# Kernel optimization log

Measured on AMD Instinct MI355X. Metric: run time of the kernel, lower is better.

## Reference

```python
import jax, jax.numpy as jnp
import numpy as np


def _make_pert(r, s):
    lin = np.linspace(-r, r, s)
    xm, ym, tm = np.meshgrid(lin, lin, lin)  # default 'xy' indexing, matches torch code
    return jnp.asarray(np.stack([xm.ravel(), ym.ravel(), tm.ravel()], axis=-1), dtype=jnp.float32)

PERTS = (_make_pert(0.01, 3), _make_pert(0.05, 5), _make_pert(0.09, 7))  # [27,3],[125,3],[343,3]

N, IN, H, HQ, FF, OUT = 4096, 3, 256, 64, 64, 3


def setup_inputs():
    key = jax.random.key(0)
    ks = jax.random.split(key, 24)

    def W(k, i, o):
        return (jax.random.normal(k, (i, o), jnp.float32) / np.sqrt(i)).astype(jnp.float32)

    one = jnp.ones((1,), jnp.float32)
    return {
        "x": jax.random.normal(ks[0], (N, 1), jnp.float32),
        "y": jax.random.normal(ks[1], (N, 1), jnp.float32),
        "t": jax.random.normal(ks[2], (N, 1), jnp.float32),
        # linear_emb: 3 -> 64 -> WaveAct -> 256
        "emb_W1": W(ks[3], IN, HQ), "emb_b1": jnp.zeros((HQ,), jnp.float32),
        "emb_wa": one, "emb_wb": one,
        "emb_W2": W(ks[4], HQ, H), "emb_b2": jnp.zeros((H,), jnp.float32),
        # multiregion_mixer: 4 -> 8 -> WaveAct -> 1
        "mix_W1": W(ks[5], 4, 8), "mix_b1": jnp.zeros((8,), jnp.float32),
        "mix_wa": one, "mix_wb": one,
        "mix_W2": W(ks[6], 8, 1), "mix_b2": jnp.zeros((1,), jnp.float32),
        "out_W0": W(ks[7], H, FF), "out_b0": jnp.zeros((FF,), jnp.float32),
        "out_wa0": one, "out_wb0": one,
        "out_Wh": jnp.stack([W(ks[8 + i], FF, FF) for i in range(3)]),
        "out_bh": jnp.zeros((3, FF), jnp.float32),
        "out_wah": jnp.ones((3, 1), jnp.float32), "out_wbh": jnp.ones((3, 1), jnp.float32),
        "out_Wf1": W(ks[11], FF, FF), "out_bf1": jnp.zeros((FF,), jnp.float32),
        "out_waf": one, "out_wbf": one,
        "out_Wf2": W(ks[12], FF, OUT), "out_bf2": jnp.zeros((OUT,), jnp.float32),
    }


def _wave(h, wa, wb):
    return wa * jnp.sin(h) + wb * jnp.cos(h)


def reference(x, y, t,
              emb_W1, emb_b1, emb_wa, emb_wb, emb_W2, emb_b2,
              mix_W1, mix_b1, mix_wa, mix_wb, mix_W2, mix_b2,
              out_W0, out_b0, out_wa0, out_wb0,
              out_Wh, out_bh, out_wah, out_wbh,
              out_Wf1, out_bf1, out_waf, out_wbf, out_Wf2, out_bf2):
    def emb(s):  # [..., 3] -> [..., 256]
        h = _wave(s @ emb_W1 + emb_b1, emb_wa, emb_wb)
        return h @ emb_W2 + emb_b2

    src = jnp.concatenate([x, y, t], axis=-1)           # [N, 3]
    feats = [emb(src)]                                   # region 1: unperturbed
    for P in PERTS:
        perturbed = src[:, None, :] + P[None, :, :]      # [N, P, 3]
        feats.append(emb(perturbed).mean(axis=1))        # [N, 256]
    stacked = jnp.stack(feats, axis=-1)                  # [N, 256, 4] (== permute(0,2,1) of stack dim=1)

    m = _wave(stacked @ mix_W1 + mix_b1, mix_wa, mix_wb) # [N, 256, 8]
    e = (m @ mix_W2 + mix_b2)[:, :, 0]                   # [N, 256]

    h = _wave(e @ out_W0 + out_b0, out_wa0, out_wb0)     # [N, 64]
    for i in range(3):                                   # fixed num_layer-1 = 3 hidden layers
        h = _wave(h @ out_Wh[i] + out_bh[i], out_wah[i], out_wbh[i])
    h = _wave(h @ out_Wf1 + out_bf1, out_waf, out_wbf)
    return h @ out_Wf2 + out_bf2                         # [N, 3]
```

## Files before the change

kernel.cpp:

```cpp
#include <hip/hip_runtime.h>

typedef _Float16 f16;
typedef _Float16 f16x8 __attribute__((ext_vector_type(8)));
typedef float v4f __attribute__((ext_vector_type(4)));

#define WS_W2T  0
#define WS_W0T  16384
#define WS_WHT  32768
#define WS_WF1T 45056
#define WS_CDW  24576
#define WS_RPHI 24768

__global__ __launch_bounds__(256) void preprocess(
    const float* __restrict__ embW1, const float* __restrict__ embW2,
    const float* __restrict__ outW0, const float* __restrict__ outWh,
    const float* __restrict__ outWf1,
    const float* __restrict__ embwa, const float* __restrict__ embwb,
    const float* __restrict__ mixwa, const float* __restrict__ mixwb,
    const float* __restrict__ outwa0, const float* __restrict__ outwb0,
    const float* __restrict__ outwah, const float* __restrict__ outwbh,
    const float* __restrict__ outwaf, const float* __restrict__ outwbf,
    f16* __restrict__ wsh)
{
    const int g = blockIdx.x * 256 + threadIdx.x;
    if (g < 16384) {
        const int c = g >> 6, k = g & 63;
        wsh[WS_W2T + g] = (f16)embW2[k*256 + c];
    } else if (g < 32768) {
        const int i = g - 16384;
        const int f = i >> 8, k = i & 255;
        wsh[WS_W0T + i] = (f16)outW0[k*64 + f];
    } else if (g < 45056) {
        const int i = g - 32768;
        const int l = i >> 12, f = (i >> 6) & 63, k = i & 63;
        wsh[WS_WHT + i] = (f16)outWh[l*4096 + k*64 + f];
    } else if (g < 49152) {
        const int i = g - 45056;
        const int f = i >> 6, k = i & 63;
        wsh[WS_WF1T + i] = (f16)outWf1[k*64 + f];
    } else if (g < 49344) {
        const int i = g - 49152;
        const int r = i >> 6, ch = i & 63;
        const float w0 = embW1[ch], w1 = embW1[64 + ch], w2 = embW1[128 + ch];
        float v;
        if (r == 0) {
            v = (1.f + 2.f*__cosf(0.01f*w0)) * (1.f + 2.f*__cosf(0.01f*w1))
              * (1.f + 2.f*__cosf(0.01f*w2)) * (1.f/27.f);
        } else if (r == 1) {
            v = (1.f + 2.f*(__cosf(0.025f*w0) + __cosf(0.05f*w0)))
              * (1.f + 2.f*(__cosf(0.025f*w1) + __cosf(0.05f*w1)))
              * (1.f + 2.f*(__cosf(0.025f*w2) + __cosf(0.05f*w2))) * (1.f/125.f);
        } else {
            v = (1.f + 2.f*(__cosf(0.03f*w0) + __cosf(0.06f*w0) + __cosf(0.09f*w0)))
              * (1.f + 2.f*(__cosf(0.03f*w1) + __cosf(0.06f*w1) + __cosf(0.09f*w1)))
              * (1.f + 2.f*(__cosf(0.03f*w2) + __cosf(0.06f*w2) + __cosf(0.09f*w2))) * (1.f/343.f);
        }
        ((float*)wsh)[WS_CDW + i] = v;
    } else if (g < 49360) {
        const int i = g - 49344;
        const int p = i >> 1;
        float wa, wb;
        switch (p) {
            case 0: wa = embwa[0];  wb = embwb[0];  break;
            case 1: wa = mixwa[0];  wb = mixwb[0];  break;
            case 2: wa = outwa0[0]; wb = outwb0[0]; break;
            case 3: case 4: case 5: wa = outwah[p-3]; wb = outwbh[p-3]; break;
            default: wa = outwaf[0]; wb = outwbf[0]; break;
        }
        const float v = (i & 1) ? atan2f(wb, wa) : sqrtf(wa*wa + wb*wb);
        ((float*)wsh)[WS_RPHI + p*2 + (i & 1)] = v;
    }
}

__global__ __launch_bounds__(256, 4) void model_mfma(
    const float* __restrict__ x, const float* __restrict__ y, const float* __restrict__ t,
    const float* __restrict__ embW1, const float* __restrict__ embb1,
    const float* __restrict__ embb2,
    const float* __restrict__ mixW1, const float* __restrict__ mixb1,
    const float* __restrict__ mixW2, const float* __restrict__ mixb2,
    const float* __restrict__ outb0, const float* __restrict__ outbh,
    const float* __restrict__ outbf1,
    const float* __restrict__ outWf2, const float* __restrict__ outbf2,
    const f16* __restrict__ wsh,
    float* __restrict__ out, int N)
{
    __shared__ __attribute__((aligned(16))) f16 sA[16*72];
    __shared__ __attribute__((aligned(16))) f16 sE[16*264];
    __shared__ __attribute__((aligned(16))) f16 sH[2][16*72];
    __shared__ float sHf[4*65];

    const int tid  = threadIdx.x;
    const int lane = tid & 63;
    const int wv   = tid >> 6;
    const int n0   = blockIdx.x * 4;
    const float* rphi = (const float*)wsh + WS_RPHI;

    {
        const int k = lane, sq = wv;
        const float w0 = embW1[k], w1 = embW1[64+k], w2 = embW1[128+k];
        const float b1 = embb1[k];
        const float* Cw = (const float*)wsh + WS_CDW;
        const float c1 = Cw[k], c2 = Cw[64+k], c3 = Cw[128+k];
        const int ns = (n0 + sq < N) ? (n0 + sq) : (N - 1);
        const float u = fmaf(x[ns], w0, fmaf(y[ns], w1, fmaf(t[ns], w2, b1)));
        const float sv = rphi[0] * __sinf(u + rphi[1]);
        f16* row = sA + (sq*4)*72 + k;
        row[0]   = (f16)sv;
        row[72]  = (f16)(sv*c1);
        row[144] = (f16)(sv*c2);
        row[216] = (f16)(sv*c3);
    }
    __syncthreads();

    const int l15 = lane & 15, qb = lane >> 4;

    {
        const f16x8 af0 = *(const f16x8*)(sA + l15*72 + qb*8);
        const f16x8 af1 = *(const f16x8*)(sA + l15*72 + 32 + qb*8);
        const float mR = rphi[2], mP = rphi[3], mb2v = mixb2[0];
        #pragma unroll
        for (int nt = 0; nt < 4; ++nt) {
            const int cb = wv*64 + nt*16;
            const f16x8 bf0 = *(const f16x8*)(wsh + WS_W2T + (cb + l15)*64 + qb*8);
            const f16x8 bf1 = *(const f16x8*)(wsh + WS_W2T + (cb + l15)*64 + 32 + qb*8);
            v4f acc = {0.f, 0.f, 0.f, 0.f};
            acc = __builtin_amdgcn_mfma_f32_16x16x32_f16(af0, bf0, acc, 0, 0, 0);
            acc = __builtin_amdgcn_mfma_f32_16x16x32_f16(af1, bf1, acc, 0, 0, 0);
            const int c = cb + l15;
            const float b2c = embb2[c];
            const float s0 = acc[0]+b2c, s1 = acc[1]+b2c, s2 = acc[2]+b2c, s3 = acc[3]+b2c;
            float ev = mb2v;
            #pragma unroll
            for (int j = 0; j < 8; ++j) {
                float p = fmaf(s0, mixW1[j],
                          fmaf(s1, mixW1[8+j],
                          fmaf(s2, mixW1[16+j],
                          fmaf(s3, mixW1[24+j], mixb1[j]))));
                ev = fmaf(mR*__sinf(p + mP), mixW2[j], ev);
            }
            sE[qb*264 + c] = (f16)ev;
        }
    }
    __syncthreads();

    const int fme = wv*16 + l15;

    {
        v4f acc = {0.f, 0.f, 0.f, 0.f};
        const f16* Ae   = sE + l15*264 + qb*8;
        const f16* W0Tg = wsh + WS_W0T + fme*256 + qb*8;
        #pragma unroll
        for (int kt = 0; kt < 8; ++kt) {
            const f16x8 af = *(const f16x8*)(Ae + kt*32);
            const f16x8 bf = *(const f16x8*)(W0Tg + kt*32);
            acc = __builtin_amdgcn_mfma_f32_16x16x32_f16(af, bf, acc, 0, 0, 0);
        }
        if (qb == 0) {
            const float b0 = outb0[fme], R = rphi[4], P = rphi[5];
            #pragma unroll
            for (int r = 0; r < 4; ++r)
                sH[0][r*72 + fme] = (f16)(R*__sinf(acc[r] + b0 + P));
        }
    }
    __syncthreads();

    int cur = 0;
    #pragma unroll
    for (int i = 0; i < 4; ++i) {
        const f16* Wg = (i < 3) ? (wsh + WS_WHT + i*4096) : (wsh + WS_WF1T);
        v4f acc = {0.f, 0.f, 0.f, 0.f};
        #pragma unroll
        for (int kt = 0; kt < 2; ++kt) {
            const f16x8 af = *(const f16x8*)(sH[cur] + l15*72 + kt*32 + qb*8);
            const f16x8 bf = *(const f16x8*)(Wg + fme*64 + kt*32 + qb*8);
            acc = __builtin_amdgcn_mfma_f32_16x16x32_f16(af, bf, acc, 0, 0, 0);
        }
        if (qb == 0) {
            float bias, R, P;
            if (i < 3) { bias = outbh[i*64 + fme]; R = rphi[6+2*i]; P = rphi[7+2*i]; }
            else       { bias = outbf1[fme];       R = rphi[12];    P = rphi[13]; }
            #pragma unroll
            for (int r = 0; r < 4; ++r) {
                const float v = R*__sinf(acc[r] + bias + P);
                if (i < 3) sH[cur^1][r*72 + fme] = (f16)v;
                else       sHf[r*65 + fme] = v;
            }
        }
        __syncthreads();
        cur ^= 1;
    }

    if (tid < 12) {
        const int s = tid / 3, o = tid - s*3;
        float a = outbf2[o];
        #pragma unroll 16
        for (int k = 0; k < 64; ++k)
            a = fmaf(sHf[s*65 + k], outWf2[k*3 + o], a);
        const int gn = n0 + s;
        if (gn < N) out[gn*3 + o] = a;
    }
}

extern "C" void kernel_launch(void* const* d_in, const int* in_sizes, int n_in,
                              void* d_out, int out_size, void* d_ws, size_t ws_size,
                              hipStream_t stream) {
    const float* x      = (const float*)d_in[0];
    const float* y      = (const float*)d_in[1];
    const float* t      = (const float*)d_in[2];
    const float* embW1  = (const float*)d_in[3];
    const float* embb1  = (const float*)d_in[4];
    const float* embwa  = (const float*)d_in[5];
    const float* embwb  = (const float*)d_in[6];
    const float* embW2  = (const float*)d_in[7];
    const float* embb2  = (const float*)d_in[8];
    const float* mixW1  = (const float*)d_in[9];
    const float* mixb1  = (const float*)d_in[10];
    const float* mixwa  = (const float*)d_in[11];
    const float* mixwb  = (const float*)d_in[12];
    const float* mixW2  = (const float*)d_in[13];
    const float* mixb2  = (const float*)d_in[14];
    const float* outW0  = (const float*)d_in[15];
    const float* outb0  = (const float*)d_in[16];
    const float* outwa0 = (const float*)d_in[17];
    const float* outwb0 = (const float*)d_in[18];
    const float* outWh  = (const float*)d_in[19];
    const float* outbh  = (const float*)d_in[20];
    const float* outwah = (const float*)d_in[21];
    const float* outwbh = (const float*)d_in[22];
    const float* outWf1 = (const float*)d_in[23];
    const float* outbf1 = (const float*)d_in[24];
    const float* outwaf = (const float*)d_in[25];
    const float* outwbf = (const float*)d_in[26];
    const float* outWf2 = (const float*)d_in[27];
    const float* outbf2 = (const float*)d_in[28];
    float* out = (float*)d_out;
    f16* wsh = (f16*)d_ws;

    const int N = in_sizes[0];

    preprocess<<<193, 256, 0, stream>>>(embW1, embW2, outW0, outWh, outWf1,
                                        embwa, embwb, mixwa, mixwb,
                                        outwa0, outwb0, outwah, outwbh,
                                        outwaf, outwbf, wsh);

    const int blocks = (N + 3) / 4;
    model_mfma<<<blocks, 256, 0, stream>>>(
        x, y, t,
        embW1, embb1, embb2,
        mixW1, mixb1, mixW2, mixb2,
        outb0, outbh, outbf1, outWf2, outbf2,
        wsh, out, N);
}
```

Measured before the change: 126.3 us.

## Run each 4-sample block with a single wavefront instead of four

Shrinks the main kernel's block from 256 threads to one 64-thread wavefront, so that one wave loops over all column tiles that four waves used to share. This is meant to remove cross-wave barrier cost and cut per-block setup overhead, since the syncthreads now cover only a single wave. In exchange, each wave does four times the serial MFMA and sin work and the per-block critical path gets longer. Occupancy now depends on how many small blocks can be resident per CU.

```diff
diff --git a/kernel.cpp b/kernel.cpp
--- a/kernel.cpp
+++ b/kernel.cpp
@@ -57,7 +57,7 @@
         }
         ((float*)wsh)[WS_CDW + i] = v;
     } else if (g < 49360) {
-        const int i = g - 49344;
+        const int i = g - 49152 - 192;
         const int p = i >> 1;
         float wa, wb;
         switch (p) {
@@ -72,7 +72,7 @@
     }
 }
 
-__global__ __launch_bounds__(256, 4) void model_mfma(
+__global__ __launch_bounds__(64) void model_mfma(
     const float* __restrict__ x, const float* __restrict__ y, const float* __restrict__ t,
     const float* __restrict__ embW1, const float* __restrict__ embb1,
     const float* __restrict__ embb2,
@@ -89,26 +89,28 @@
     __shared__ __attribute__((aligned(16))) f16 sH[2][16*72];
     __shared__ float sHf[4*65];
 
-    const int tid  = threadIdx.x;
-    const int lane = tid & 63;
-    const int wv   = tid >> 6;
+    const int lane = threadIdx.x;
     const int n0   = blockIdx.x * 4;
     const float* rphi = (const float*)wsh + WS_RPHI;
 
     {
-        const int k = lane, sq = wv;
+        const int k = lane;
         const float w0 = embW1[k], w1 = embW1[64+k], w2 = embW1[128+k];
         const float b1 = embb1[k];
         const float* Cw = (const float*)wsh + WS_CDW;
         const float c1 = Cw[k], c2 = Cw[64+k], c3 = Cw[128+k];
-        const int ns = (n0 + sq < N) ? (n0 + sq) : (N - 1);
-        const float u = fmaf(x[ns], w0, fmaf(y[ns], w1, fmaf(t[ns], w2, b1)));
-        const float sv = rphi[0] * __sinf(u + rphi[1]);
-        f16* row = sA + (sq*4)*72 + k;
-        row[0]   = (f16)sv;
-        row[72]  = (f16)(sv*c1);
-        row[144] = (f16)(sv*c2);
-        row[216] = (f16)(sv*c3);
+        const float Re = rphi[0], Pe = rphi[1];
+        #pragma unroll
+        for (int sq = 0; sq < 4; ++sq) {
+            const int ns = (n0 + sq < N) ? (n0 + sq) : (N - 1);
+            const float u = fmaf(x[ns], w0, fmaf(y[ns], w1, fmaf(t[ns], w2, b1)));
+            const float sv = Re * __sinf(u + Pe);
+            f16* row = sA + (sq*4)*72 + k;
+            row[0]   = (f16)sv;
+            row[72]  = (f16)(sv*c1);
+            row[144] = (f16)(sv*c2);
+            row[216] = (f16)(sv*c3);
+        }
     }
     __syncthreads();
 
@@ -118,9 +120,9 @@
         const f16x8 af0 = *(const f16x8*)(sA + l15*72 + qb*8);
         const f16x8 af1 = *(const f16x8*)(sA + l15*72 + 32 + qb*8);
         const float mR = rphi[2], mP = rphi[3], mb2v = mixb2[0];
-        #pragma unroll
-        for (int nt = 0; nt < 4; ++nt) {
-            const int cb = wv*64 + nt*16;
+        #pragma unroll 4
+        for (int nt = 0; nt < 16; ++nt) {
+            const int cb = nt*16;
             const f16x8 bf0 = *(const f16x8*)(wsh + WS_W2T + (cb + l15)*64 + qb*8);
             const f16x8 bf1 = *(const f16x8*)(wsh + WS_W2T + (cb + l15)*64 + 32 + qb*8);
             v4f acc = {0.f, 0.f, 0.f, 0.f};
@@ -143,23 +145,26 @@
     }
     __syncthreads();
 
-    const int fme = wv*16 + l15;
-
     {
-        v4f acc = {0.f, 0.f, 0.f, 0.f};
-        const f16* Ae   = sE + l15*264 + qb*8;
-        const f16* W0Tg = wsh + WS_W0T + fme*256 + qb*8;
+        const float R = rphi[4], P = rphi[5];
         #pragma unroll
-        for (int kt = 0; kt < 8; ++kt) {
-            const f16x8 af = *(const f16x8*)(Ae + kt*32);
-            const f16x8 bf = *(const f16x8*)(W0Tg + kt*32);
-            acc = __builtin_amdgcn_mfma_f32_16x16x32_f16(af, bf, acc, 0, 0, 0);
-        }
-        if (qb == 0) {
-            const float b0 = outb0[fme], R = rphi[4], P = rphi[5];
+        for (int ft = 0; ft < 4; ++ft) {
+            const int fme = ft*16 + l15;
+            v4f acc = {0.f, 0.f, 0.f, 0.f};
+            const f16* Ae   = sE + l15*264 + qb*8;
+            const f16* W0Tg = wsh + WS_W0T + fme*256 + qb*8;
             #pragma unroll
-            for (int r = 0; r < 4; ++r)
-                sH[0][r*72 + fme] = (f16)(R*__sinf(acc[r] + b0 + P));
+            for (int kt = 0; kt < 8; ++kt) {
+                const f16x8 af = *(const f16x8*)(Ae + kt*32);
+                const f16x8 bf = *(const f16x8*)(W0Tg + kt*32);
+                acc = __builtin_amdgcn_mfma_f32_16x16x32_f16(af, bf, acc, 0, 0, 0);
+            }
+            if (qb == 0) {
+                const float b0 = outb0[fme];
+                #pragma unroll
+                for (int r = 0; r < 4; ++r)
+                    sH[0][r*72 + fme] = (f16)(R*__sinf(acc[r] + b0 + P));
+            }
         }
     }
     __syncthreads();
@@ -168,30 +173,34 @@
     #pragma unroll
     for (int i = 0; i < 4; ++i) {
         const f16* Wg = (i < 3) ? (wsh + WS_WHT + i*4096) : (wsh + WS_WF1T);
-        v4f acc = {0.f, 0.f, 0.f, 0.f};
         #pragma unroll
-        for (int kt = 0; kt < 2; ++kt) {
-            const f16x8 af = *(const f16x8*)(sH[cur] + l15*72 + kt*32 + qb*8);
-            const f16x8 bf = *(const f16x8*)(Wg + fme*64 + kt*32 + qb*8);
-            acc = __builtin_amdgcn_mfma_f32_16x16x32_f16(af, bf, acc, 0, 0, 0);
-        }
-        if (qb == 0) {
-            float bias, R, P;
-            if (i < 3) { bias = outbh[i*64 + fme]; R = rphi[6+2*i]; P = rphi[7+2*i]; }
-            else       { bias = outbf1[fme];       R = rphi[12];    P = rphi[13]; }
+        for (int ft = 0; ft < 4; ++ft) {
+            const int fme = ft*16 + l15;
+            v4f acc = {0.f, 0.f, 0.f, 0.f};
             #pragma unroll
-            for (int r = 0; r < 4; ++r) {
-                const float v = R*__sinf(acc[r] + bias + P);
-                if (i < 3) sH[cur^1][r*72 + fme] = (f16)v;
-                else       sHf[r*65 + fme] = v;
+            for (int kt = 0; kt < 2; ++kt) {
+                const f16x8 af = *(const f16x8*)(sH[cur] + l15*72 + kt*32 + qb*8);
+                const f16x8 bf = *(const f16x8*)(Wg + fme*64 + kt*32 + qb*8);
+                acc = __builtin_amdgcn_mfma_f32_16x16x32_f16(af, bf, acc, 0, 0, 0);
+            }
+            if (qb == 0) {
+                float bias, R, P;
+                if (i < 3) { bias = outbh[i*64 + fme]; R = rphi[6+2*i]; P = rphi[7+2*i]; }
+                else       { bias = outbf1[fme];       R = rphi[12];    P = rphi[13]; }
+                #pragma unroll
+                for (int r = 0; r < 4; ++r) {
+                    const float v = R*__sinf(acc[r] + bias + P);
+                    if (i < 3) sH[cur^1][r*72 + fme] = (f16)v;
+                    else       sHf[r*65 + fme] = v;
+                }
             }
         }
         __syncthreads();
         cur ^= 1;
     }
 
-    if (tid < 12) {
-        const int s = tid / 3, o = tid - s*3;
+    if (lane < 12) {
+        const int s = lane / 3, o = lane - s*3;
         float a = outbf2[o];
         #pragma unroll 16
         for (int k = 0; k < 64; ++k)
@@ -244,7 +253,7 @@
                                         outwaf, outwbf, wsh);
 
     const int blocks = (N + 3) / 4;
-    model_mfma<<<blocks, 256, 0, stream>>>(
+    model_mfma<<<blocks, 64, 0, stream>>>(
         x, y, t,
         embW1, embb1, embb2,
         mixW1, mixb1, mixW2, mixb2,
```

New measurement: 133.5 us. +5.7%, slower.
